# Performance work log

Measured on AMD Instinct MI355X. Metric: run time of the kernel, lower is better.

Reference implementation:

```python
import jax, jax.numpy as jnp
import numpy as np

NUM_NEG = 5
VOCAB = 50257
BATCH = 4096


def setup_inputs() -> dict:
    key = jax.random.key(0)
    k1, k2, k3 = jax.random.split(key, 3)
    input = jax.nn.log_softmax(jax.random.normal(k1, (BATCH, VOCAB), dtype=jnp.float32), axis=-1)
    freqs = jax.random.uniform(k2, (VOCAB,), dtype=jnp.float32, minval=1e-3, maxval=1.0)
    target = jax.random.randint(k3, (BATCH,), 0, VOCAB, dtype=jnp.int32)
    return {"input": input, "freqs": freqs, "target": target}


def _neg_sample_weights(freqs, target, num_neg, key):
    # distr = L2-normalized freq^0.75 (L2 norm doesn't change categorical sampling,
    # kept for faithfulness to nn.functional.normalize in the torch code)
    distr = freqs ** 0.75
    distr = distr / jnp.linalg.norm(distr)
    vocab = freqs.shape[0]
    # positive counts: weights[w] += 1 for each w in target
    pos_counts = jnp.zeros((vocab,), dtype=jnp.float32).at[target].add(1.0)
    # rejection sampling "while w in positives: resample" is equivalent to
    # sampling from the distribution with positives masked out -- vectorized here
    masked = jnp.where(pos_counts > 0, 0.0, distr)
    neg = jax.random.categorical(key, jnp.log(masked), shape=(num_neg,))
    weights = pos_counts.at[neg].add(1.0)
    return weights


def reference(input, freqs, target):
    key = jax.random.key(42)
    weights = _neg_sample_weights(freqs, target, NUM_NEG, key)
    # nll_loss with per-class weights, mean reduction:
    # loss = -sum_i w[t_i] * input[i, t_i] / sum_i w[t_i]
    batch = input.shape[0]
    w_t = weights[target]                              # [B]
    picked = input[jnp.arange(batch), target]          # [B]
    return -(w_t * picked).sum() / w_t.sum()
```

## Files before the change

### kernel.cpp

```cpp
#include <hip/hip_runtime.h>


#define NEG_VOCAB 50257
#define NEG_HIST_WORDS ((NEG_VOCAB + 1) / 2)

__global__ __launch_bounds__(1024) void negloss_kernel(
    const float* __restrict__ input,
    const int* __restrict__ target,
    float* __restrict__ out,
    int B, int V) {
    __shared__ unsigned int hist[NEG_HIST_WORDS];
    __shared__ float s_num[16];
    __shared__ float s_den[16];

    const int tid = threadIdx.x;
    const int T = blockDim.x;

    for (int v = tid; v < NEG_HIST_WORDS; v += T) hist[v] = 0u;
    __syncthreads();

    for (int i = tid; i < B; i += T) {
        int t = target[i];
        atomicAdd(&hist[t >> 1], 1u << ((t & 1) << 4));
    }
    __syncthreads();

    float num = 0.f, den = 0.f;
    for (int i = tid; i < B; i += T) {
        int t = target[i];
        unsigned int p = hist[t >> 1];
        float w = (float)((p >> ((t & 1) << 4)) & 0xFFFFu);
        float x = input[(long long)i * (long long)V + t];
        num += w * x;
        den += w;
    }

#pragma unroll
    for (int off = 32; off > 0; off >>= 1) {
        num += __shfl_down(num, off, 64);
        den += __shfl_down(den, off, 64);
    }
    const int wave = tid >> 6;
    if ((tid & 63) == 0) { s_num[wave] = num; s_den[wave] = den; }
    __syncthreads();

    if (tid == 0) {
        float N = 0.f, D = 0.f;
        const int nw = T >> 6;
        for (int w = 0; w < nw; ++w) { N += s_num[w]; D += s_den[w]; }
        out[0] = -N / D;
    }
}

extern "C" void kernel_launch(void* const* d_in, const int* in_sizes, int n_in,
                              void* d_out, int out_size, void* d_ws, size_t ws_size,
                              hipStream_t stream) {
    const float* input = (const float*)d_in[0];
    const int* target = (const int*)d_in[2];
    float* out = (float*)d_out;

    const int V = in_sizes[1];
    const int B = in_sizes[2];

    negloss_kernel<<<dim3(1), dim3(1024), 0, stream>>>(input, target, out, B, V);
}
```

Measured before the change: 10.20 us.

## Split loss across vocab-chunk blocks with per-class aggregation and finalize kernel

Replaces the single-block kernel with 64 blocks of 256 threads. Each block owns one contiguous vocab chunk, scans every target with int4 loads, and counts and sums the input values for targets that fall in its chunk. The loss is then rewritten per class as num = sum of count*sum and den = sum of count squared. A small second kernel combines the per-block partials from the workspace. This spreads the LDS zeroing and the scattered input gathers over many compute units, at the cost of an extra launch, every block re-reading the full target array, and nondeterministic float atomics.

```diff
diff --git a/kernel.cpp b/kernel.cpp
--- a/kernel.cpp
+++ b/kernel.cpp
@@ -1,30 +1,94 @@
 #include <hip/hip_runtime.h>
 
 
-#define NEG_VOCAB 50257
-#define NEG_HIST_WORDS ((NEG_VOCAB + 1) / 2)
+#define NEG_G 64
+#define NEG_T 256
+#define NEG_VOCAB_MAX 50304
 
-__global__ __launch_bounds__(1024) void negloss_kernel(
+__global__ __launch_bounds__(NEG_T) void negloss_main(
     const float* __restrict__ input,
     const int* __restrict__ target,
-    float* __restrict__ out,
+    float* __restrict__ partials,
     int B, int V) {
-    __shared__ unsigned int hist[NEG_HIST_WORDS];
-    __shared__ float s_num[16];
-    __shared__ float s_den[16];
+    const int CHUNK = (V + NEG_G - 1) / NEG_G;
+    __shared__ unsigned int cnt[NEG_VOCAB_MAX / NEG_G];
+    __shared__ float S[NEG_VOCAB_MAX / NEG_G];
+    __shared__ float s_num[NEG_T / 64], s_den[NEG_T / 64];
 
     const int tid = threadIdx.x;
+    const int v0 = blockIdx.x * CHUNK;
+
+    for (int v = tid; v < CHUNK; v += NEG_T) { cnt[v] = 0u; S[v] = 0.f; }
+    __syncthreads();
+
+    const int4* t4 = (const int4*)target;
+    for (int idx = tid; idx < B / 4; idx += NEG_T) {
+        int4 tv = t4[idx];
+        int t_arr[4] = {tv.x, tv.y, tv.z, tv.w};
+        const int base_i = idx * 4;
+#pragma unroll
+        for (int k = 0; k < 4; ++k) {
+            int local = t_arr[k] - v0;
+            if ((unsigned)local < (unsigned)CHUNK) {
+                atomicAdd(&cnt[local], 1u);
+                float x = input[(long long)(base_i + k) * (long long)V + t_arr[k]];
+                atomicAdd(&S[local], x);
+            }
+        }
+    }
+    __syncthreads();
+
+    float num = 0.f, den = 0.f;
+    for (int v = tid; v < CHUNK; v += NEG_T) {
+        float c = (float)cnt[v];
+        num += c * S[v];
+        den += c * c;
+    }
+#pragma unroll
+    for (int off = 32; off > 0; off >>= 1) {
+        num += __shfl_down(num, off, 64);
+        den += __shfl_down(den, off, 64);
+    }
+    const int wave = tid >> 6;
+    if ((tid & 63) == 0) { s_num[wave] = num; s_den[wave] = den; }
+    __syncthreads();
+    if (tid == 0) {
+        float N = 0.f, D = 0.f;
+#pragma unroll
+        for (int w = 0; w < NEG_T / 64; ++w) { N += s_num[w]; D += s_den[w]; }
+        partials[2 * blockIdx.x] = N;
+        partials[2 * blockIdx.x + 1] = D;
+    }
+}
+
+__global__ __launch_bounds__(64) void negloss_finalize(
+    const float* __restrict__ partials, float* __restrict__ out) {
+    const int lane = threadIdx.x;
+    float num = partials[2 * lane];
+    float den = partials[2 * lane + 1];
+#pragma unroll
+    for (int off = 32; off > 0; off >>= 1) {
+        num += __shfl_down(num, off, 64);
+        den += __shfl_down(den, off, 64);
+    }
+    if (lane == 0) out[0] = -num / den;
+}
+
+#define NEG_HIST_WORDS ((50257 + 1) / 2)
+__global__ __launch_bounds__(1024) void negloss_single(
+    const float* __restrict__ input, const int* __restrict__ target,
+    float* __restrict__ out, int B, int V) {
+    __shared__ unsigned int hist[NEG_HIST_WORDS];
+    __shared__ float s_num[16], s_den[16];
+    const int tid = threadIdx.x;
     const int T = blockDim.x;
-
     for (int v = tid; v < NEG_HIST_WORDS; v += T) hist[v] = 0u;
     __syncthreads();
-
     for (int i = tid; i < B; i += T) {
         int t = target[i];
         atomicAdd(&hist[t >> 1], 1u << ((t & 1) << 4));
     }
     __syncthreads();
-
     float num = 0.f, den = 0.f;
     for (int i = tid; i < B; i += T) {
         int t = target[i];
@@ -34,7 +98,6 @@
         num += w * x;
         den += w;
     }
-
 #pragma unroll
     for (int off = 32; off > 0; off >>= 1) {
         num += __shfl_down(num, off, 64);
@@ -43,11 +106,9 @@
     const int wave = tid >> 6;
     if ((tid & 63) == 0) { s_num[wave] = num; s_den[wave] = den; }
     __syncthreads();
-
     if (tid == 0) {
         float N = 0.f, D = 0.f;
-        const int nw = T >> 6;
-        for (int w = 0; w < nw; ++w) { N += s_num[w]; D += s_den[w]; }
+        for (int w = 0; w < T >> 6; ++w) { N += s_num[w]; D += s_den[w]; }
         out[0] = -N / D;
     }
 }
@@ -58,9 +119,14 @@
     const float* input = (const float*)d_in[0];
     const int* target = (const int*)d_in[2];
     float* out = (float*)d_out;
-
     const int V = in_sizes[1];
     const int B = in_sizes[2];
 
-    negloss_kernel<<<dim3(1), dim3(1024), 0, stream>>>(input, target, out, B, V);
+    if (ws_size >= 2 * NEG_G * sizeof(float)) {
+        float* partials = (float*)d_ws;
+        negloss_main<<<dim3(NEG_G), dim3(NEG_T), 0, stream>>>(input, target, partials, B, V);
+        negloss_finalize<<<dim3(1), dim3(64), 0, stream>>>(partials, out);
+    } else {
+        negloss_single<<<dim3(1), dim3(1024), 0, stream>>>(input, target, out, B, V);
+    }
 }
```

After: 10.99 us. 7.7% more time.

## Split vocab histogram across cooperative blocks and reduce per-class sums algebraically

Applied to the files above, without the earlier changes.

Spreads the work over eight cooperative blocks, each owning a slice of the vocabulary. Each block bins targets into its slice, accumulating both counts and the gathered log-probabilities in shared memory. The loss terms then become sum(cnt*S) and sum(cnt^2) over classes, and a grid sync lets block 0 combine the per-block partials. This aims to shorten the single-block serial histogram and gather path. In exchange it pays for a cooperative launch and grid barrier, and it hardcodes B as 4*1024 through the int4 target load.

```diff
diff --git a/kernel.cpp b/kernel.cpp
--- a/kernel.cpp
+++ b/kernel.cpp
@@ -1,53 +1,74 @@
 #include <hip/hip_runtime.h>
+#include <hip/hip_cooperative_groups.h>
+
+namespace cg = cooperative_groups;
 
 
-#define NEG_VOCAB 50257
-#define NEG_HIST_WORDS ((NEG_VOCAB + 1) / 2)
+#define NEG_K 8
+#define NEG_T 1024
+#define NEG_CHUNK 6283
 
-__global__ __launch_bounds__(1024) void negloss_kernel(
+__global__ __launch_bounds__(NEG_T) void negloss_coop(
     const float* __restrict__ input,
     const int* __restrict__ target,
     float* __restrict__ out,
+    float* __restrict__ partials,
     int B, int V) {
-    __shared__ unsigned int hist[NEG_HIST_WORDS];
-    __shared__ float s_num[16];
-    __shared__ float s_den[16];
+    __shared__ unsigned int cnt[NEG_CHUNK];
+    __shared__ float S[NEG_CHUNK];
+    __shared__ float s_num[NEG_T / 64], s_den[NEG_T / 64];
 
     const int tid = threadIdx.x;
-    const int T = blockDim.x;
+    const int blk = blockIdx.x;
+    const int v0 = blk * NEG_CHUNK;
 
-    for (int v = tid; v < NEG_HIST_WORDS; v += T) hist[v] = 0u;
+    for (int v = tid; v < NEG_CHUNK; v += NEG_T) { cnt[v] = 0u; S[v] = 0.f; }
     __syncthreads();
 
-    for (int i = tid; i < B; i += T) {
-        int t = target[i];
-        atomicAdd(&hist[t >> 1], 1u << ((t & 1) << 4));
+    const int4 tv = ((const int4*)target)[tid];
+    const int ts[4] = {tv.x, tv.y, tv.z, tv.w};
+#pragma unroll
+    for (int k = 0; k < 4; ++k) {
+        const int local = ts[k] - v0;
+        if ((unsigned)local < (unsigned)NEG_CHUNK) {
+            atomicAdd(&cnt[local], 1u);
+            const float x = input[(long long)(4 * tid + k) * (long long)V + ts[k]];
+            atomicAdd(&S[local], x);
+        }
     }
     __syncthreads();
 
     float num = 0.f, den = 0.f;
-    for (int i = tid; i < B; i += T) {
-        int t = target[i];
-        unsigned int p = hist[t >> 1];
-        float w = (float)((p >> ((t & 1) << 4)) & 0xFFFFu);
-        float x = input[(long long)i * (long long)V + t];
-        num += w * x;
-        den += w;
+    for (int v = tid; v < NEG_CHUNK; v += NEG_T) {
+        const float c = (float)cnt[v];
+        num = fmaf(c, S[v], num);
+        den = fmaf(c, c, den);
     }
-
 #pragma unroll
     for (int off = 32; off > 0; off >>= 1) {
         num += __shfl_down(num, off, 64);
         den += __shfl_down(den, off, 64);
     }
-    const int wave = tid >> 6;
-    if ((tid & 63) == 0) { s_num[wave] = num; s_den[wave] = den; }
+    if ((tid & 63) == 0) { s_num[tid >> 6] = num; s_den[tid >> 6] = den; }
     __syncthreads();
 
     if (tid == 0) {
         float N = 0.f, D = 0.f;
-        const int nw = T >> 6;
-        for (int w = 0; w < nw; ++w) { N += s_num[w]; D += s_den[w]; }
+#pragma unroll
+        for (int w = 0; w < NEG_T / 64; ++w) { N += s_num[w]; D += s_den[w]; }
+        __hip_atomic_store(&partials[2 * blk],     N, __ATOMIC_RELEASE, __HIP_MEMORY_SCOPE_AGENT);
+        __hip_atomic_store(&partials[2 * blk + 1], D, __ATOMIC_RELEASE, __HIP_MEMORY_SCOPE_AGENT);
+    }
+
+    cg::this_grid().sync();
+
+    if (blk == 0 && tid == 0) {
+        float N = 0.f, D = 0.f;
+#pragma unroll
+        for (int b2 = 0; b2 < NEG_K; ++b2) {
+            N += __hip_atomic_load(&partials[2 * b2],     __ATOMIC_ACQUIRE, __HIP_MEMORY_SCOPE_AGENT);
+            D += __hip_atomic_load(&partials[2 * b2 + 1], __ATOMIC_ACQUIRE, __HIP_MEMORY_SCOPE_AGENT);
+        }
         out[0] = -N / D;
     }
 }
@@ -58,9 +79,12 @@
     const float* input = (const float*)d_in[0];
     const int* target = (const int*)d_in[2];
     float* out = (float*)d_out;
+    float* partials = (float*)d_ws;
+    int V = in_sizes[1];
+    int B = in_sizes[2];
 
-    const int V = in_sizes[1];
-    const int B = in_sizes[2];
-
-    negloss_kernel<<<dim3(1), dim3(1024), 0, stream>>>(input, target, out, B, V);
+    void* args[] = {(void*)&input, (void*)&target, (void*)&out,
+                    (void*)&partials, (void*)&B, (void*)&V};
+    hipLaunchCooperativeKernel((const void*)negloss_coop,
+                               dim3(NEG_K), dim3(NEG_T), args, 0, stream);
 }
```

After: 35.43 us. 3.47x slower.
